# Performance work log

Measured on AMD Instinct MI355X. Metric: run time of the kernel, lower is better.

The kernel has to match this reference:

```python
import jax, jax.numpy as jnp
import numpy as np

N, D, H, C, E, I, L, B = 16000, 128, 2, 128, 256000, 512, 2, 64
NTYPES = 10


def setup_inputs() -> dict:
    key = jax.random.key(0)
    ks = jax.random.split(key, 20)
    s = 0.05
    inp = {
        'x': jax.random.normal(ks[0], (N, D), jnp.float32),
        'hetro_emb': jax.random.normal(ks[1], (NTYPES, D), jnp.float32) * s,
        'Wq': jax.random.normal(ks[2], (D, H * C), jnp.float32) * s,
        'bq': jnp.zeros((H * C,), jnp.float32),
        'Wk': jax.random.normal(ks[3], (D, H * C), jnp.float32) * s,
        'bk': jnp.zeros((H * C,), jnp.float32),
        'Wv': jax.random.normal(ks[4], (D, H * C), jnp.float32) * s,
        'bv': jnp.zeros((H * C,), jnp.float32),
        'We': jax.random.normal(ks[5], (D, H * C), jnp.float32) * s,
        'Wskip': jax.random.normal(ks[6], (D, C), jnp.float32) * s,
        'bskip': jnp.zeros((C,), jnp.float32),
        'ln_gamma': jnp.ones((L, D), jnp.float32),
        'ln_beta': jnp.zeros((L, D), jnp.float32),
        'ffn_w1': jax.random.normal(ks[7], (L, D, I), jnp.float32) * s,
        'ffn_b1': jnp.zeros((L, I), jnp.float32),
        'ffn_w2': jax.random.normal(ks[8], (L, I, D), jnp.float32) * s,
        'ffn_b2': jnp.zeros((L, D), jnp.float32),
        'edge_index': jax.random.randint(ks[9], (2, E), 0, N, jnp.int64),
        'edge_type': jax.random.randint(ks[10], (E,), 0, NTYPES, jnp.int64),
        'mask_idx': jax.random.randint(ks[11], (B,), 0, N, jnp.int64),
    }
    return inp


def _layer_norm(h, gamma, beta, eps=1e-6):
    mu = h.mean(-1, keepdims=True)
    var = ((h - mu) ** 2).mean(-1, keepdims=True)
    return (h - mu) * jax.lax.rsqrt(var + eps) * gamma + beta


def reference(x, hetro_emb, Wq, bq, Wk, bk, Wv, bv, We, Wskip, bskip,
              ln_gamma, ln_beta, ffn_w1, ffn_b1, ffn_w2, ffn_b2,
              edge_index, edge_type, mask_idx):
    src, dst = edge_index[0], edge_index[1]  # messages flow src(j) -> dst(i)
    edge_attr_raw = hetro_emb[edge_type]     # [E, D], computed once outside the layer loop
    scale = 1.0 / jnp.sqrt(jnp.asarray(C, x.dtype))

    h = x
    pre = h
    for l in range(L):
        # shared GRANConv weights across layers (same module appended n_gcn_layer times)
        q = (h @ Wq + bq).reshape(-1, H, C)
        k = (h @ Wk + bk).reshape(-1, H, C)
        v = (h @ Wv + bv).reshape(-1, H, C)
        eproj = (edge_attr_raw @ We).reshape(-1, H, C)  # [E, H, C]
        kj = k[src] + eproj                              # [E, H, C]
        logits = (q[dst] * kj).sum(-1) * scale           # [E, H]
        # segment softmax over destination nodes
        m = jax.ops.segment_max(logits, dst, num_segments=N)  # [N, H]
        a = jnp.exp(logits - m[dst])
        ssum = jax.ops.segment_sum(a, dst, num_segments=N)
        alpha = a / (ssum[dst] + 1e-16)                  # [E, H]
        msg = (v[src] + eproj) * alpha[..., None]        # [E, H, C]
        agg = jax.ops.segment_sum(msg, dst, num_segments=N)  # [N, H, C]
        out = agg.mean(1) + (h @ Wskip + bskip)          # concat=False -> head mean; root skip
        # residual + LN + FFN (no activation between the two FFN linears)
        hres = out + pre
        hln = _layer_norm(hres, ln_gamma[l], ln_beta[l])
        h = (hln @ ffn_w1[l] + ffn_b1[l]) @ ffn_w2[l] + ffn_b2[l]
        pre = h

    return h[mask_idx]  # [B, D]
```

## Files before the change

kernel.cpp:

```cpp
#include <hip/hip_runtime.h>
#include <hip/hip_bf16.h>
#include <math.h>

#define DD 128
#define QW 896
#define CAP 128
#define NB 125
#define BCAP 4096

typedef _Float16 f16x8 __attribute__((ext_vector_type(8)));
typedef _Float16 f16x2 __attribute__((ext_vector_type(2)));
typedef float f32x4 __attribute__((ext_vector_type(4)));

__device__ __forceinline__ float fdot2f(f16x2 a, f16x2 b, float c) {
#if __has_builtin(__builtin_amdgcn_fdot2)
  return __builtin_amdgcn_fdot2(a, b, c, false);
#else
  return fmaf((float)a[0], (float)b[0], fmaf((float)a[1], (float)b[1], c));
#endif
}

__global__ __launch_bounds__(256) void csr_count(const int* __restrict__ edst,
                                                 int* __restrict__ bcnt, int E) {
  __shared__ int h[NB];
  const int tid = threadIdx.x;
  if (tid < NB) h[tid] = 0;
  __syncthreads();
  const int e0 = blockIdx.x * 2048;
  for (int k = 0; k < 8; ++k) {
    int e = e0 + k * 256 + tid;
    if (e < E) atomicAdd(&h[edst[e] >> 7], 1);
  }
  __syncthreads();
  if (tid < NB && h[tid]) atomicAdd(&bcnt[tid], h[tid]);
}

__global__ __launch_bounds__(128) void csr_scan(const int* __restrict__ bcnt,
                                                int* __restrict__ bbase,
                                                int* __restrict__ bcursor,
                                                int* __restrict__ offs, int E, int Nn) {
  __shared__ int sc[128];
  const int tid = threadIdx.x;
  sc[tid] = (tid < NB) ? bcnt[tid] : 0;
  __syncthreads();
  for (int d = 1; d < 128; d <<= 1) {
    int t = (tid >= d) ? sc[tid - d] : 0;
    __syncthreads();
    sc[tid] += t;
    __syncthreads();
  }
  const int excl = tid ? sc[tid - 1] : 0;
  if (tid < NB) { bbase[tid] = excl; bcursor[tid] = excl; }
  if (tid == 0) { bbase[NB] = E; offs[Nn] = E; }
}

__global__ __launch_bounds__(256) void csr_scatter(const int* __restrict__ edst,
                                                   const int* __restrict__ esrc,
                                                   const int* __restrict__ etyp,
                                                   int* __restrict__ bcursor,
                                                   unsigned* __restrict__ ebuf, int E) {
  __shared__ int h[NB], cur[NB];
  const int tid = threadIdx.x;
  if (tid < NB) h[tid] = 0;
  __syncthreads();
  const int e0 = blockIdx.x * 2048;
  int dd[8];
  for (int k = 0; k < 8; ++k) {
    int e = e0 + k * 256 + tid;
    dd[k] = (e < E) ? edst[e] : -1;
    if (dd[k] >= 0) atomicAdd(&h[dd[k] >> 7], 1);
  }
  __syncthreads();
  if (tid < NB && h[tid]) cur[tid] = atomicAdd(&bcursor[tid], h[tid]);
  __syncthreads();
  for (int k = 0; k < 8; ++k) {
    int e = e0 + k * 256 + tid;
    if (dd[k] >= 0) {
      int pos = atomicAdd(&cur[dd[k] >> 7], 1);
      ebuf[pos] = (unsigned)esrc[e] | ((unsigned)etyp[e] << 14) |
                  ((unsigned)(dd[k] & 127) << 18);
    }
  }
}

__global__ __launch_bounds__(256) void csr_fine(const unsigned* __restrict__ ebuf,
                                                const int* __restrict__ bbase,
                                                unsigned* __restrict__ epk,
                                                int* __restrict__ offs,
                                                int* __restrict__ dcnt) {
  __shared__ unsigned sed[BCAP];
  __shared__ unsigned sout[BCAP];
  __shared__ int fh[128], sc[128], fc[128], hb[64];
  const int b = blockIdx.x, tid = threadIdx.x;
  const int base = bbase[b], cnt = bbase[b + 1] - base;
  for (int idx = tid; idx < cnt; idx += 256) sed[idx] = ebuf[base + idx];
  if (tid < 128) fh[tid] = 0;
  if (tid < 64) hb[tid] = 0;
  __syncthreads();
  for (int idx = tid; idx < cnt; idx += 256) atomicAdd(&fh[(sed[idx] >> 18) & 127], 1);
  __syncthreads();
  if (tid < 128) sc[tid] = fh[tid];
  __syncthreads();
  for (int d = 1; d < 128; d <<= 1) {
    int t = (tid < 128 && tid >= d) ? sc[tid - d] : 0;
    __syncthreads();
    if (tid < 128) sc[tid] += t;
    __syncthreads();
  }
  if (tid < 128) {
    const int excl = tid ? sc[tid - 1] : 0;
    offs[b * 128 + tid] = base + excl;
    fc[tid] = excl;
    atomicAdd(&hb[min(fh[tid], 63)], 1);
  }
  __syncthreads();
  if (tid < 64 && hb[tid]) atomicAdd(&dcnt[tid], hb[tid]);
  for (int idx = tid; idx < cnt; idx += 256) {
    const unsigned v = sed[idx];
    const int pos = atomicAdd(&fc[(v >> 18) & 127], 1);
    sout[pos] = (v & 0x3FFF) | (((v >> 14) & 0xF) << 18);
  }
  __syncthreads();
  for (int idx = tid; idx < cnt; idx += 256) epk[base + idx] = sout[idx];
}

__global__ __launch_bounds__(64) void deg_scan(const int* __restrict__ dcnt,
                                               int* __restrict__ dcur) {
  const int t = threadIdx.x;
  int s = 0;
  for (int d = t + 1; d < 64; ++d) s += dcnt[d];
  dcur[t] = s;
}

__global__ __launch_bounds__(256) void deg_order(const int* __restrict__ offs,
                                                 int* __restrict__ dcur,
                                                 int* __restrict__ order, int Nn) {
  __shared__ int h[64], cbase[64];
  const int tid = threadIdx.x;
  const int i = blockIdx.x * 256 + tid;
  if (tid < 64) h[tid] = 0;
  __syncthreads();
  int bk = -1;
  if (i < Nn) {
    bk = min(offs[i + 1] - offs[i], 63);
    atomicAdd(&h[bk], 1);
  }
  __syncthreads();
  if (tid < 64) {
    const int c = h[tid];
    cbase[tid] = c ? atomicAdd(&dcur[tid], c) : 0;
    h[tid] = 0;
  }
  __syncthreads();
  if (bk >= 0) {
    const int pos = cbase[bk] + atomicAdd(&h[bk], 1);
    order[pos] = i;
  }
}

__global__ __launch_bounds__(256) void pp_cast(
    const float* __restrict__ Wq, const float* __restrict__ Wk,
    const float* __restrict__ Wv, const float* __restrict__ Wsk,
    const float* __restrict__ bq, const float* __restrict__ bk,
    const float* __restrict__ bv, const float* __restrict__ bsk,
    const float* __restrict__ hemb, const float* __restrict__ We,
    const float* __restrict__ x,
    const float* __restrict__ fw1, const float* __restrict__ fb1,
    const float* __restrict__ fw2, const float* __restrict__ fb2,
    _Float16* __restrict__ WcatT, float* __restrict__ Wcat, float* __restrict__ bcat,
    _Float16* __restrict__ epth, _Float16* __restrict__ xh,
    _Float16* __restrict__ fw1h,
    float* __restrict__ bfv, float* __restrict__ bzero, int Nn) {
  int t = blockIdx.x * 256 + threadIdx.x;
  if (t < 256) {
    int l = t >> 7, j = t & 127;
    const float* b1 = fb1 + l * 512;
    const float* w2 = fw2 + (size_t)l * 65536 + j;
    float s0 = fb2[l * 128 + j], s1 = 0.f, s2 = 0.f, s3 = 0.f;
    for (int k = 0; k < 512; k += 4) {
      s0 = fmaf(b1[k], w2[(size_t)k * 128], s0);
      s1 = fmaf(b1[k + 1], w2[(size_t)(k + 1) * 128], s1);
      s2 = fmaf(b1[k + 2], w2[(size_t)(k + 2) * 128], s2);
      s3 = fmaf(b1[k + 3], w2[(size_t)(k + 3) * 128], s3);
    }
    bfv[t] = ((s0 + s1) + (s2 + s3));
    return;
  }
  t -= 256;
  if (t < 2560) {
    int ty = t >> 8, col = t & 255;
    float s0 = 0.f, s1 = 0.f, s2 = 0.f, s3 = 0.f;
    const float* hr = hemb + ty * 128;
    for (int c = 0; c < 128; c += 4) {
      s0 = fmaf(hr[c], We[c * 256 + col], s0);
      s1 = fmaf(hr[c + 1], We[(c + 1) * 256 + col], s1);
      s2 = fmaf(hr[c + 2], We[(c + 2) * 256 + col], s2);
      s3 = fmaf(hr[c + 3], We[(c + 3) * 256 + col], s3);
    }
    epth[t] = (_Float16)((s0 + s1) + (s2 + s3));
    return;
  }
  t -= 2560;
  if (t < 114688) {
    int n = t >> 7, k = t & 127;
    float v;
    if (n < 256) v = Wq[k * 256 + n];
    else if (n < 512) v = Wk[k * 256 + (n - 256)];
    else if (n < 768) v = Wv[k * 256 + (n - 512)];
    else v = Wsk[k * 128 + (n - 768)];
    WcatT[t] = (_Float16)v;
    Wcat[k * 896 + n] = v;
    return;
  }
  t -= 114688;
  if (t < 896) {
    float v;
    if (t < 256) v = bq[t];
    else if (t < 512) v = bk[t - 256];
    else if (t < 768) v = bv[t - 512];
    else v = bsk[t - 768];
    bcat[t] = v;
    return;
  }
  t -= 896;
  if (t < 1024) { bzero[t] = 0.f; return; }
  t -= 1024;
  if (t < 16384) {
    float4 v0 = *reinterpret_cast<const float4*>(fw1 + (size_t)t * 8);
    float4 v1 = *reinterpret_cast<const float4*>(fw1 + (size_t)t * 8 + 4);
    f16x8 o;
    o[0] = (_Float16)v0.x; o[1] = (_Float16)v0.y; o[2] = (_Float16)v0.z; o[3] = (_Float16)v0.w;
    o[4] = (_Float16)v1.x; o[5] = (_Float16)v1.y; o[6] = (_Float16)v1.z; o[7] = (_Float16)v1.w;
    *reinterpret_cast<f16x8*>(fw1h + (size_t)t * 8) = o;
    return;
  }
  t -= 16384;
  if (t < Nn * 16) {
    float4 v0 = *reinterpret_cast<const float4*>(x + (size_t)t * 8);
    float4 v1 = *reinterpret_cast<const float4*>(x + (size_t)t * 8 + 4);
    f16x8 o;
    o[0] = (_Float16)v0.x; o[1] = (_Float16)v0.y; o[2] = (_Float16)v0.z; o[3] = (_Float16)v0.w;
    o[4] = (_Float16)v1.x; o[5] = (_Float16)v1.y; o[6] = (_Float16)v1.z; o[7] = (_Float16)v1.w;
    *reinterpret_cast<f16x8*>(xh + (size_t)t * 8) = o;
  }
}

__global__ __launch_bounds__(256) void tr_fw2(const float* __restrict__ fw2,
                                              _Float16* __restrict__ fw2Th) {
  __shared__ _Float16 tile[64][65];
  const int l = blockIdx.z;
  const int k0 = blockIdx.x * 64, j0 = blockIdx.y * 64;
  const size_t base = (size_t)l * 65536;
  const int tid = threadIdx.x;
  for (int idx = tid; idx < 4096; idx += 256) {
    int r = idx >> 6, c = idx & 63;
    tile[r][c] = (_Float16)fw2[base + (size_t)(k0 + r) * 128 + j0 + c];
  }
  __syncthreads();
  for (int idx = tid; idx < 4096; idx += 256) {
    int r = idx >> 6, c = idx & 63;
    fw2Th[base + (size_t)(j0 + r) * 512 + k0 + c] = tile[c][r];
  }
}

__global__ __launch_bounds__(256) void pp_bmid(const float* __restrict__ bfv,
                                               const float* __restrict__ Wcat,
                                               const float* __restrict__ bcat,
                                               float* __restrict__ bmid) {
  int t = blockIdx.x * 256 + threadIdx.x;
  if (t >= 1024) return;
  if (t < 128) { bmid[t] = bfv[t]; return; }
  int n = t - 128;
  float s0 = bcat[n], s1 = 0.f, s2 = 0.f, s3 = 0.f;
  for (int c = 0; c < 128; c += 4) {
    s0 = fmaf(bfv[c], Wcat[c * 896 + n], s0);
    s1 = fmaf(bfv[c + 1], Wcat[(c + 1) * 896 + n], s1);
    s2 = fmaf(bfv[c + 2], Wcat[(c + 2) * 896 + n], s2);
    s3 = fmaf(bfv[c + 3], Wcat[(c + 3) * 896 + n], s3);
  }
  bmid[t] = ((s0 + s1) + (s2 + s3));
}

__global__ __launch_bounds__(256) void wf_gemm(const _Float16* __restrict__ fw1h,
                                               const _Float16* __restrict__ fw2Th,
                                               float* __restrict__ Wf,
                                               _Float16* __restrict__ Wfh,
                                               _Float16* __restrict__ BtMid0) {
  const int z = blockIdx.z;
  const _Float16* A = fw1h + z * 65536;
  const _Float16* Bt = fw2Th + z * 65536;
  const int tid = threadIdx.x;
  const int wid = tid >> 6, lane = tid & 63;
  const int wr = wid >> 1, wc = wid & 1;
  const int il = lane & 15, g = lane >> 4;
  const int row0 = wr * 64, col0 = wc * 64;
  const _Float16* Ap = A + (size_t)(row0 + il) * 512 + 8 * g;
  const _Float16* Bp = Bt + (size_t)(col0 + il) * 512 + 8 * g;
  f32x4 acc[4][4];
#pragma unroll
  for (int a = 0; a < 4; ++a)
#pragma unroll
    for (int b = 0; b < 4; ++b) acc[a][b] = (f32x4){0.f, 0.f, 0.f, 0.f};
  for (int k0 = 0; k0 < 512; k0 += 32) {
    f16x8 af[4], bf[4];
#pragma unroll
    for (int f = 0; f < 4; ++f) {
      af[f] = *reinterpret_cast<const f16x8*>(Ap + (size_t)(f * 16) * 512 + k0);
      bf[f] = *reinterpret_cast<const f16x8*>(Bp + (size_t)(f * 16) * 512 + k0);
    }
#pragma unroll
    for (int fi = 0; fi < 4; ++fi)
#pragma unroll
      for (int fj = 0; fj < 4; ++fj)
        acc[fi][fj] = __builtin_amdgcn_mfma_f32_16x16x32_f16(af[fi], bf[fj], acc[fi][fj], 0, 0, 0);
  }
#pragma unroll
  for (int fj = 0; fj < 4; ++fj) {
    const int col = col0 + fj * 16 + il;
#pragma unroll
    for (int fi = 0; fi < 4; ++fi) {
#pragma unroll
      for (int i = 0; i < 4; ++i) {
        const int row = row0 + fi * 16 + g * 4 + i;
        const float v = acc[fi][fj][i];
        Wf[z * 16384 + row * 128 + col] = v;
        if (z == 0) {
          Wfh[row * 128 + col] = (_Float16)v;
          BtMid0[col * 128 + row] = (_Float16)v;
        }
      }
    }
  }
}

template <bool HAS_CFH, bool HAS_CH, bool HAS_CHT>
__global__ __launch_bounds__(256) void gemm_tn_f16(const _Float16* __restrict__ A,
                                                   const _Float16* __restrict__ Bt,
                                                   const float* __restrict__ bias,
                                                   _Float16* __restrict__ Cfh, int NF,
                                                   _Float16* __restrict__ Ch, int choff, int ldh,
                                                   _Float16* __restrict__ ChT, int ldt,
                                                   int M, int N, int K) {
  const int tid = threadIdx.x;
  const int wid = tid >> 6, lane = tid & 63;
  const int wr = wid >> 1, wc = wid & 1;
  const int il = lane & 15, g = lane >> 4;
  const int row0 = blockIdx.y * 128 + wr * 64;
  const int col0 = blockIdx.x * 128 + wc * 64;
  const _Float16* Ap = A + (size_t)(row0 + il) * K + 8 * g;
  const _Float16* Bp = Bt + (size_t)(col0 + il) * K + 8 * g;
  f32x4 acc[4][4];
#pragma unroll
  for (int a = 0; a < 4; ++a)
#pragma unroll
    for (int b = 0; b < 4; ++b) acc[a][b] = (f32x4){0.f, 0.f, 0.f, 0.f};
  for (int k0 = 0; k0 < K; k0 += 32) {
    f16x8 af[4], bf[4];
#pragma unroll
    for (int f = 0; f < 4; ++f) {
      af[f] = *reinterpret_cast<const f16x8*>(Ap + (size_t)(f * 16) * K + k0);
      bf[f] = *reinterpret_cast<const f16x8*>(Bp + (size_t)(f * 16) * K + k0);
    }
#pragma unroll
    for (int fi = 0; fi < 4; ++fi)
#pragma unroll
      for (int fj = 0; fj < 4; ++fj)
        acc[fi][fj] = __builtin_amdgcn_mfma_f32_16x16x32_f16(af[fi], bf[fj], acc[fi][fj], 0, 0, 0);
  }
#pragma unroll
  for (int fj = 0; fj < 4; ++fj) {
    const int col = col0 + fj * 16 + il;
    const float b = bias[col];
#pragma unroll
    for (int fi = 0; fi < 4; ++fi) {
#pragma unroll
      for (int i = 0; i < 4; ++i) {
        const int row = row0 + fi * 16 + g * 4 + i;
        const float v = acc[fi][fj][i] + b;
        if constexpr (HAS_CFH) { if (col < NF) Cfh[(size_t)row * NF + col] = (_Float16)v; }
        if constexpr (HAS_CH) { if (col >= choff) Ch[(size_t)row * ldh + (col - choff)] = (_Float16)v; }
        if constexpr (HAS_CHT) { ChT[(size_t)col * ldt + row] = (_Float16)v; }
      }
    }
  }
}

__global__ __launch_bounds__(256) void node_attn_ln_kernel(
    const _Float16* __restrict__ QKVSh, const _Float16* __restrict__ epth,
    const _Float16* __restrict__ hpre,
    const int* __restrict__ offs, const unsigned* __restrict__ epk,
    const int* __restrict__ order,
    const float* __restrict__ gamma, const float* __restrict__ beta,
    _Float16* __restrict__ hlnh, int Nn) {
  __shared__ float sl0[4][CAP], sl1[4][CAP];
  __shared__ unsigned spk[4][CAP];
  __shared__ float sqe[4][2][10];
  __shared__ __align__(16) _Float16 elds[2560];
  const int tid = threadIdx.x;
  for (int t = tid; t < 1280; t += 256)
    reinterpret_cast<unsigned*>(elds)[t] = reinterpret_cast<const unsigned*>(epth)[t];
  __syncthreads();
  const int w = tid >> 6, lane = tid & 63;
  const int i = order[blockIdx.x * 4 + w];
  const int sub = lane >> 5;
  const int r = lane & 31;
  const int half = r >> 4;
  const int co = r << 3;
  const float scale = 0.08838834764831845f;
  f16x8 qh = *reinterpret_cast<const f16x8*>(QKVSh + (size_t)i * QW + co);
  const f16x2* q2 = reinterpret_cast<const f16x2*>(&qh);
#pragma unroll
  for (int ty = 0; ty < 10; ++ty) {
    f16x8 ev = *reinterpret_cast<const f16x8*>(elds + (ty << 8) + co);
    const f16x2* e2 = reinterpret_cast<const f16x2*>(&ev);
    float s = 0.f;
#pragma unroll
    for (int p2 = 0; p2 < 4; ++p2) s = fdot2f(q2[p2], e2[p2], s);
    s += __shfl_xor(s, 1); s += __shfl_xor(s, 2);
    s += __shfl_xor(s, 4); s += __shfl_xor(s, 8);
    if (lane < 32 && (r & 15) == 0) sqe[w][half][ty] = s * scale;
  }
  __threadfence_block();
  float m_me = -1e30f, s_me = 0.f;
  float acc[8] = {0.f};
  const int ebeg = offs[i], eend = offs[i + 1];
  for (int cs = ebeg; cs < eend; cs += CAP) {
    const int cnt = min(CAP, eend - cs);
    const int last = cnt - 1;
    for (int j = lane; j < cnt; j += 64) spk[w][j] = epk[cs + j];
    __threadfence_block();
    float cmax = -1e30f;
    {
      unsigned pk0 = spk[w][min(sub, last)];
      unsigned pk1 = spk[w][min(2 + sub, last)];
      f16x8 kv0 = *reinterpret_cast<const f16x8*>(QKVSh + (size_t)(pk0 & 0x3FFFF) * QW + 256 + co);
      f16x8 kv1 = *reinterpret_cast<const f16x8*>(QKVSh + (size_t)(pk1 & 0x3FFFF) * QW + 256 + co);
      int ty0 = pk0 >> 18, ty1 = pk1 >> 18;
      for (int j = 0; j < cnt; j += 2) {
        f16x8 kc = kv0;
        const int tyc = ty0;
        kv0 = kv1; ty0 = ty1;
        unsigned pkn = spk[w][min(j + 4 + sub, last)];
        ty1 = pkn >> 18;
        kv1 = *reinterpret_cast<const f16x8*>(QKVSh + (size_t)(pkn & 0x3FFFF) * QW + 256 + co);
        const f16x2* k2 = reinterpret_cast<const f16x2*>(&kc);
        float d = 0.f;
#pragma unroll
        for (int p2 = 0; p2 < 4; ++p2) d = fdot2f(q2[p2], k2[p2], d);
        d += __shfl_xor(d, 1); d += __shfl_xor(d, 2);
        d += __shfl_xor(d, 4); d += __shfl_xor(d, 8);
        d = d * scale + sqe[w][half][tyc];
        if (j + sub < cnt) {
          cmax = fmaxf(cmax, d);
          if ((r & 15) == 0) (half ? sl1 : sl0)[w][j + sub] = d;
        }
      }
    }
    cmax = fmaxf(cmax, __shfl_xor(cmax, 32));
    const float nm = fmaxf(m_me, cmax);
    const float rr = __expf(m_me - nm);
    s_me *= rr;
#pragma unroll
    for (int t = 0; t < 8; ++t) acc[t] *= rr;
    m_me = nm;
    __threadfence_block();
    {
      unsigned pk0 = spk[w][min(sub, last)];
      unsigned pk1 = spk[w][min(2 + sub, last)];
      f16x8 vv0 = *reinterpret_cast<const f16x8*>(QKVSh + (size_t)(pk0 & 0x3FFFF) * QW + 512 + co);
      f16x8 ee0 = *reinterpret_cast<const f16x8*>(elds + ((pk0 >> 18) << 8) + co);
      f16x8 vv1 = *reinterpret_cast<const f16x8*>(QKVSh + (size_t)(pk1 & 0x3FFFF) * QW + 512 + co);
      f16x8 ee1 = *reinterpret_cast<const f16x8*>(elds + ((pk1 >> 18) << 8) + co);
      const float* slme = (half ? sl1 : sl0)[w];
      float ls = 0.f;
      for (int j = 0; j < cnt; j += 2) {
        f16x8 vc = vv0, ec = ee0;
        vv0 = vv1; ee0 = ee1;
        unsigned pkn = spk[w][min(j + 4 + sub, last)];
        vv1 = *reinterpret_cast<const f16x8*>(QKVSh + (size_t)(pkn & 0x3FFFF) * QW + 512 + co);
        ee1 = *reinterpret_cast<const f16x8*>(elds + ((pkn >> 18) << 8) + co);
        const int jc = j + sub;
        float e = 0.f;
        if (jc < cnt) e = __expf(slme[jc] - m_me);
        ls += e;
#pragma unroll
        for (int t = 0; t < 8; ++t) acc[t] = fmaf((float)vc[t] + (float)ec[t], e, acc[t]);
      }
      s_me += ls;
    }
  }
  const float s_tot = s_me + __shfl_xor(s_me, 32);
  const float invme = 1.f / (s_tot + 1e-16f);
  float g[8];
#pragma unroll
  for (int t = 0; t < 8; ++t) {
    float a = acc[t] + __shfl_xor(acc[t], 32);
    a *= invme;
    g[t] = 0.5f * (a + __shfl_xor(a, 16));
  }
  const int cm = (r & 15) << 3;
  f16x8 sk = *reinterpret_cast<const f16x8*>(QKVSh + (size_t)i * QW + 768 + cm);
  f16x8 pr = *reinterpret_cast<const f16x8*>(hpre + (size_t)i * DD + cm);
  float xv[8];
#pragma unroll
  for (int t = 0; t < 8; ++t) xv[t] = g[t] + (float)sk[t] + (float)pr[t];
  float sm = 0.f;
#pragma unroll
  for (int t = 0; t < 8; ++t) sm += xv[t];
  sm += __shfl_xor(sm, 1); sm += __shfl_xor(sm, 2);
  sm += __shfl_xor(sm, 4); sm += __shfl_xor(sm, 8);
  const float mu = sm * (1.f / 128.f);
  float dx[8], vvs = 0.f;
#pragma unroll
  for (int t = 0; t < 8; ++t) { dx[t] = xv[t] - mu; vvs += dx[t] * dx[t]; }
  vvs += __shfl_xor(vvs, 1); vvs += __shfl_xor(vvs, 2);
  vvs += __shfl_xor(vvs, 4); vvs += __shfl_xor(vvs, 8);
  const float rstd = rsqrtf(vvs * (1.f / 128.f) + 1e-6f);
  if (lane < 16) {
    float4 gm0 = *reinterpret_cast<const float4*>(gamma + cm);
    float4 gm1 = *reinterpret_cast<const float4*>(gamma + cm + 4);
    float4 bt0 = *reinterpret_cast<const float4*>(beta + cm);
    float4 bt1 = *reinterpret_cast<const float4*>(beta + cm + 4);
    f16x8 o;
    o[0] = (_Float16)(dx[0] * rstd * gm0.x + bt0.x);
    o[1] = (_Float16)(dx[1] * rstd * gm0.y + bt0.y);
    o[2] = (_Float16)(dx[2] * rstd * gm0.z + bt0.z);
    o[3] = (_Float16)(dx[3] * rstd * gm0.w + bt0.w);
    o[4] = (_Float16)(dx[4] * rstd * gm1.x + bt1.x);
    o[5] = (_Float16)(dx[5] * rstd * gm1.y + bt1.y);
    o[6] = (_Float16)(dx[6] * rstd * gm1.z + bt1.z);
    o[7] = (_Float16)(dx[7] * rstd * gm1.w + bt1.w);
    *reinterpret_cast<f16x8*>(hlnh + (size_t)i * DD + cm) = o;
  }
}

__global__ __launch_bounds__(128) void final_kernel(const _Float16* __restrict__ hlnh1,
                                                    const float* __restrict__ Wf,
                                                    const float* __restrict__ bfv,
                                                    const int* __restrict__ midx,
                                                    float* __restrict__ out) {
  __shared__ float rowv[128];
  const int b = blockIdx.x, j = threadIdx.x;
  const int row = midx[b];
  rowv[j] = (float)hlnh1[(size_t)row * DD + j];
  __syncthreads();
  const float* w1 = Wf + 16384 + j;
  float s = bfv[128 + j];
#pragma unroll 4
  for (int c = 0; c < 128; ++c) s = fmaf(rowv[c], w1[c * 128], s);
  out[b * DD + j] = s;
}

extern "C" void kernel_launch(void* const* d_in, const int* in_sizes, int n_in,
                              void* d_out, int out_size, void* d_ws, size_t ws_size,
                              hipStream_t stream) {
  const float* x    = (const float*)d_in[0];
  const float* hemb = (const float*)d_in[1];
  const float* Wq   = (const float*)d_in[2];
  const float* bq   = (const float*)d_in[3];
  const float* Wk   = (const float*)d_in[4];
  const float* bk   = (const float*)d_in[5];
  const float* Wv   = (const float*)d_in[6];
  const float* bv   = (const float*)d_in[7];
  const float* We   = (const float*)d_in[8];
  const float* Wsk  = (const float*)d_in[9];
  const float* bsk  = (const float*)d_in[10];
  const float* lng  = (const float*)d_in[11];
  const float* lnb  = (const float*)d_in[12];
  const float* fw1  = (const float*)d_in[13];
  const float* fb1  = (const float*)d_in[14];
  const float* fw2  = (const float*)d_in[15];
  const float* fb2  = (const float*)d_in[16];
  const int* eidx   = (const int*)d_in[17];
  const int* etyp   = (const int*)d_in[18];
  const int* midx   = (const int*)d_in[19];

  const int Nn = in_sizes[0] / DD;
  const int E = in_sizes[18];

  const int* esrc = eidx;
  const int* edst = eidx + E;

  char* p = (char*)d_ws;
  auto alloc = [&](size_t bytes) -> void* {
    void* r = (void*)p;
    p += (bytes + 255) & ~(size_t)255;
    return r;
  };
  _Float16* QKVSh = (_Float16*)alloc((size_t)Nn * QW * 2);
  _Float16* xh    = (_Float16*)alloc((size_t)Nn * DD * 2);
  _Float16* hln0  = (_Float16*)alloc((size_t)Nn * DD * 2);
  _Float16* hln1  = (_Float16*)alloc((size_t)Nn * DD * 2);
  _Float16* h1h   = (_Float16*)alloc((size_t)Nn * DD * 2);
  _Float16* WcatT = (_Float16*)alloc((size_t)QW * DD * 2);
  float*    Wcat  = (float*)alloc((size_t)DD * QW * 4);
  float*    bcat  = (float*)alloc(QW * 4);
  _Float16* epth  = (_Float16*)alloc(2560 * 2);
  _Float16* fw1h  = (_Float16*)alloc((size_t)2 * DD * 512 * 2);
  _Float16* fw2Th = (_Float16*)alloc((size_t)2 * DD * 512 * 2);
  float*    Wf    = (float*)alloc(2 * 128 * 128 * 4);
  _Float16* Wfh   = (_Float16*)alloc(128 * 128 * 2);
  float*    bfv   = (float*)alloc(256 * 4);
  float*    bzero = (float*)alloc(1024 * 4);
  _Float16* BtMid = (_Float16*)alloc((size_t)1024 * 128 * 2);
  float*    bmid  = (float*)alloc(1024 * 4);
  int* offs   = (int*)alloc((size_t)(Nn + 1) * 4);
  int* bcnt   = (int*)alloc((NB + 1) * 4);
  int* bbase  = (int*)alloc((NB + 1) * 4);
  int* bcursor= (int*)alloc((NB + 1) * 4);
  int* dcnt   = (int*)alloc(64 * 4);
  int* dcur   = (int*)alloc(64 * 4);
  int* order  = (int*)alloc((size_t)Nn * 4);
  unsigned* ebuf = (unsigned*)alloc((size_t)E * 4);
  unsigned* epk  = (unsigned*)alloc((size_t)E * 4);

  hipMemsetAsync(bcnt, 0, (NB + 1) * sizeof(int), stream);
  hipMemsetAsync(dcnt, 0, 64 * sizeof(int), stream);
  csr_count<<<(E + 2047) / 2048, 256, 0, stream>>>(edst, bcnt, E);
  csr_scan<<<1, 128, 0, stream>>>(bcnt, bbase, bcursor, offs, E, Nn);
  csr_scatter<<<(E + 2047) / 2048, 256, 0, stream>>>(edst, esrc, etyp, bcursor, ebuf, E);
  csr_fine<<<NB, 256, 0, stream>>>(ebuf, bbase, epk, offs, dcnt);
  deg_scan<<<1, 64, 0, stream>>>(dcnt, dcur);
  deg_order<<<(Nn + 255) / 256, 256, 0, stream>>>(offs, dcur, order, Nn);

  const int pc_threads = 256 + 2560 + 114688 + 896 + 1024 + 16384 + Nn * 16;
  pp_cast<<<(pc_threads + 255) / 256, 256, 0, stream>>>(
      Wq, Wk, Wv, Wsk, bq, bk, bv, bsk, hemb, We, x, fw1, fb1, fw2, fb2,
      WcatT, Wcat, bcat, epth, xh, fw1h, bfv, bzero, Nn);
  tr_fw2<<<dim3(8, 2, 2), 256, 0, stream>>>(fw2, fw2Th);
  pp_bmid<<<4, 256, 0, stream>>>(bfv, Wcat, bcat, bmid);
  wf_gemm<<<dim3(1, 1, 2), 256, 0, stream>>>(fw1h, fw2Th, Wf, Wfh, BtMid);
  gemm_tn_f16<false, false, true><<<dim3(7, 1), 256, 0, stream>>>(
      Wfh, WcatT, bzero, nullptr, 0, nullptr, 0, 0, BtMid + 16384, 128, 128, 896, 128);

  gemm_tn_f16<false, true, false><<<dim3(QW / 128, Nn / 128), 256, 0, stream>>>(
      xh, WcatT, bcat, nullptr, 0, QKVSh, 0, QW, nullptr, 0, Nn, QW, DD);
  node_attn_ln_kernel<<<Nn / 4, 256, 0, stream>>>(QKVSh, epth, xh, offs, epk, order,
                                                  lng, lnb, hln0, Nn);
  gemm_tn_f16<true, true, false><<<dim3(1024 / 128, Nn / 128), 256, 0, stream>>>(
      hln0, BtMid, bmid, h1h, 128, QKVSh, 128, QW, nullptr, 0, Nn, 1024, DD);
  node_attn_ln_kernel<<<Nn / 4, 256, 0, stream>>>(QKVSh, epth, h1h, offs, epk, order,
                                                  lng + DD, lnb + DD, hln1, Nn);
  final_kernel<<<64, 128, 0, stream>>>(hln1, Wf, bfv, midx, (float*)d_out);
}
```

Measured before the change: 257.4 us.

## Use single-pass online softmax in attention; drop memsets and fold transpose into cast kernel

The node attention kernel now runs a single-pass online softmax. It loads K and V together per edge straight from global memory and rescales lazily, replacing the two-pass chunked scheme that staged logits and packed edges in shared memory. The two half-waves' partial max/sum are merged with a rescale at the end. Separately, the global atomics and memsets for the bucket and degree counts become per-block partial arrays summed in the scan kernels, and the fw2 transpose kernel is folded into extra blocks of pp_cast, cutting launches. The risk is more divergent exponent and rescale work per edge, plus register pressure from prefetching both K and V.

New measurement: 274.9 us. +6.8%, slower.

```diff
diff --git a/kernel.cpp b/kernel.cpp
--- a/kernel.cpp
+++ b/kernel.cpp
@@ -4,7 +4,6 @@
 
 #define DD 128
 #define QW 896
-#define CAP 128
 #define NB 125
 #define BCAP 4096
 
@@ -21,7 +20,7 @@
 }
 
 __global__ __launch_bounds__(256) void csr_count(const int* __restrict__ edst,
-                                                 int* __restrict__ bcnt, int E) {
+                                                 int* __restrict__ bparts, int E) {
   __shared__ int h[NB];
   const int tid = threadIdx.x;
   if (tid < NB) h[tid] = 0;
@@ -32,16 +31,18 @@
     if (e < E) atomicAdd(&h[edst[e] >> 7], 1);
   }
   __syncthreads();
-  if (tid < NB && h[tid]) atomicAdd(&bcnt[tid], h[tid]);
-}
-
-__global__ __launch_bounds__(128) void csr_scan(const int* __restrict__ bcnt,
+  if (tid < 128) bparts[blockIdx.x * 128 + tid] = (tid < NB) ? h[tid] : 0;
+}
+
+__global__ __launch_bounds__(128) void csr_scan(const int* __restrict__ bparts, int nblk,
                                                 int* __restrict__ bbase,
                                                 int* __restrict__ bcursor,
                                                 int* __restrict__ offs, int E, int Nn) {
   __shared__ int sc[128];
   const int tid = threadIdx.x;
-  sc[tid] = (tid < NB) ? bcnt[tid] : 0;
+  int s = 0;
+  for (int b = 0; b < nblk; ++b) s += bparts[b * 128 + tid];
+  sc[tid] = (tid < NB) ? s : 0;
   __syncthreads();
   for (int d = 1; d < 128; d <<= 1) {
     int t = (tid >= d) ? sc[tid - d] : 0;
@@ -87,7 +88,7 @@
                                                 const int* __restrict__ bbase,
                                                 unsigned* __restrict__ epk,
                                                 int* __restrict__ offs,
-                                                int* __restrict__ dcnt) {
+                                                int* __restrict__ dparts) {
   __shared__ unsigned sed[BCAP];
   __shared__ unsigned sout[BCAP];
   __shared__ int fh[128], sc[128], fc[128], hb[64];
@@ -114,7 +115,7 @@
     atomicAdd(&hb[min(fh[tid], 63)], 1);
   }
   __syncthreads();
-  if (tid < 64 && hb[tid]) atomicAdd(&dcnt[tid], hb[tid]);
+  if (tid < 64) dparts[b * 64 + tid] = hb[tid];
   for (int idx = tid; idx < cnt; idx += 256) {
     const unsigned v = sed[idx];
     const int pos = atomicAdd(&fc[(v >> 18) & 127], 1);
@@ -124,12 +125,17 @@
   for (int idx = tid; idx < cnt; idx += 256) epk[base + idx] = sout[idx];
 }
 
-__global__ __launch_bounds__(64) void deg_scan(const int* __restrict__ dcnt,
+__global__ __launch_bounds__(64) void deg_scan(const int* __restrict__ dparts, int nblk,
                                                int* __restrict__ dcur) {
+  __shared__ int tot[64];
   const int t = threadIdx.x;
   int s = 0;
-  for (int d = t + 1; d < 64; ++d) s += dcnt[d];
-  dcur[t] = s;
+  for (int b = 0; b < nblk; ++b) s += dparts[b * 64 + t];
+  tot[t] = s;
+  __syncthreads();
+  int acc = 0;
+  for (int d = t + 1; d < 64; ++d) acc += tot[d];
+  dcur[t] = acc;
 }
 
 __global__ __launch_bounds__(256) void deg_order(const int* __restrict__ offs,
@@ -169,8 +175,26 @@
     const float* __restrict__ fw2, const float* __restrict__ fb2,
     _Float16* __restrict__ WcatT, float* __restrict__ Wcat, float* __restrict__ bcat,
     _Float16* __restrict__ epth, _Float16* __restrict__ xh,
-    _Float16* __restrict__ fw1h,
-    float* __restrict__ bfv, float* __restrict__ bzero, int Nn) {
+    _Float16* __restrict__ fw1h, _Float16* __restrict__ fw2Th,
+    float* __restrict__ bfv, float* __restrict__ bzero, int Nn, int nb0) {
+  __shared__ _Float16 tile[64][65];
+  if (blockIdx.x >= nb0) {
+    const int tb = blockIdx.x - nb0;
+    const int l = tb >> 4, r2 = tb & 15;
+    const int k0 = (r2 >> 1) << 6, j0 = (r2 & 1) << 6;
+    const size_t base = (size_t)l * 65536;
+    const int tid = threadIdx.x;
+    for (int idx = tid; idx < 4096; idx += 256) {
+      int rr = idx >> 6, cc = idx & 63;
+      tile[rr][cc] = (_Float16)fw2[base + (size_t)(k0 + rr) * 128 + j0 + cc];
+    }
+    __syncthreads();
+    for (int idx = tid; idx < 4096; idx += 256) {
+      int rr = idx >> 6, cc = idx & 63;
+      fw2Th[base + (size_t)(j0 + rr) * 512 + k0 + cc] = tile[cc][rr];
+    }
+    return;
+  }
   int t = blockIdx.x * 256 + threadIdx.x;
   if (t < 256) {
     int l = t >> 7, j = t & 127;
@@ -242,24 +266,6 @@
     o[0] = (_Float16)v0.x; o[1] = (_Float16)v0.y; o[2] = (_Float16)v0.z; o[3] = (_Float16)v0.w;
     o[4] = (_Float16)v1.x; o[5] = (_Float16)v1.y; o[6] = (_Float16)v1.z; o[7] = (_Float16)v1.w;
     *reinterpret_cast<f16x8*>(xh + (size_t)t * 8) = o;
-  }
-}
-
-__global__ __launch_bounds__(256) void tr_fw2(const float* __restrict__ fw2,
-                                              _Float16* __restrict__ fw2Th) {
-  __shared__ _Float16 tile[64][65];
-  const int l = blockIdx.z;
-  const int k0 = blockIdx.x * 64, j0 = blockIdx.y * 64;
-  const size_t base = (size_t)l * 65536;
-  const int tid = threadIdx.x;
-  for (int idx = tid; idx < 4096; idx += 256) {
-    int r = idx >> 6, c = idx & 63;
-    tile[r][c] = (_Float16)fw2[base + (size_t)(k0 + r) * 128 + j0 + c];
-  }
-  __syncthreads();
-  for (int idx = tid; idx < 4096; idx += 256) {
-    int r = idx >> 6, c = idx & 63;
-    fw2Th[base + (size_t)(j0 + r) * 512 + k0 + c] = tile[c][r];
   }
 }
 
@@ -392,8 +398,6 @@
     const int* __restrict__ order,
     const float* __restrict__ gamma, const float* __restrict__ beta,
     _Float16* __restrict__ hlnh, int Nn) {
-  __shared__ float sl0[4][CAP], sl1[4][CAP];
-  __shared__ unsigned spk[4][CAP];
   __shared__ float sqe[4][2][10];
   __shared__ __align__(16) _Float16 elds[2560];
   const int tid = threadIdx.x;
@@ -424,78 +428,63 @@
   float m_me = -1e30f, s_me = 0.f;
   float acc[8] = {0.f};
   const int ebeg = offs[i], eend = offs[i + 1];
-  for (int cs = ebeg; cs < eend; cs += CAP) {
-    const int cnt = min(CAP, eend - cs);
-    const int last = cnt - 1;
-    for (int j = lane; j < cnt; j += 64) spk[w][j] = epk[cs + j];
-    __threadfence_block();
-    float cmax = -1e30f;
-    {
-      unsigned pk0 = spk[w][min(sub, last)];
-      unsigned pk1 = spk[w][min(2 + sub, last)];
-      f16x8 kv0 = *reinterpret_cast<const f16x8*>(QKVSh + (size_t)(pk0 & 0x3FFFF) * QW + 256 + co);
-      f16x8 kv1 = *reinterpret_cast<const f16x8*>(QKVSh + (size_t)(pk1 & 0x3FFFF) * QW + 256 + co);
-      int ty0 = pk0 >> 18, ty1 = pk1 >> 18;
-      for (int j = 0; j < cnt; j += 2) {
-        f16x8 kc = kv0;
-        const int tyc = ty0;
-        kv0 = kv1; ty0 = ty1;
-        unsigned pkn = spk[w][min(j + 4 + sub, last)];
-        ty1 = pkn >> 18;
-        kv1 = *reinterpret_cast<const f16x8*>(QKVSh + (size_t)(pkn & 0x3FFFF) * QW + 256 + co);
-        const f16x2* k2 = reinterpret_cast<const f16x2*>(&kc);
-        float d = 0.f;
-#pragma unroll
-        for (int p2 = 0; p2 < 4; ++p2) d = fdot2f(q2[p2], k2[p2], d);
-        d += __shfl_xor(d, 1); d += __shfl_xor(d, 2);
-        d += __shfl_xor(d, 4); d += __shfl_xor(d, 8);
-        d = d * scale + sqe[w][half][tyc];
-        if (j + sub < cnt) {
-          cmax = fmaxf(cmax, d);
-          if ((r & 15) == 0) (half ? sl1 : sl0)[w][j + sub] = d;
-        }
+  if (ebeg < eend) {
+    const int last = eend - 1;
+    unsigned pk0 = epk[min(ebeg + sub, last)];
+    unsigned pk1 = epk[min(ebeg + 2 + sub, last)];
+    const _Float16* r0p = QKVSh + (size_t)(pk0 & 0x3FFFF) * QW;
+    const _Float16* r1p = QKVSh + (size_t)(pk1 & 0x3FFFF) * QW;
+    f16x8 kv0 = *reinterpret_cast<const f16x8*>(r0p + 256 + co);
+    f16x8 vv0 = *reinterpret_cast<const f16x8*>(r0p + 512 + co);
+    f16x8 kv1 = *reinterpret_cast<const f16x8*>(r1p + 256 + co);
+    f16x8 vv1 = *reinterpret_cast<const f16x8*>(r1p + 512 + co);
+    for (int j = ebeg; j < eend; j += 2) {
+      f16x8 kc = kv0, vc = vv0;
+      const unsigned pkc = pk0;
+      kv0 = kv1; vv0 = vv1; pk0 = pk1;
+      pk1 = epk[min(j + 4 + sub, last)];
+      const _Float16* rp = QKVSh + (size_t)(pk1 & 0x3FFFF) * QW;
+      kv1 = *reinterpret_cast<const f16x8*>(rp + 256 + co);
+      vv1 = *reinterpret_cast<const f16x8*>(rp + 512 + co);
+      const int tyc = pkc >> 18;
+      const f16x2* k2 = reinterpret_cast<const f16x2*>(&kc);
+      float d = 0.f;
+#pragma unroll
+      for (int p2 = 0; p2 < 4; ++p2) d = fdot2f(q2[p2], k2[p2], d);
+      d += __shfl_xor(d, 1); d += __shfl_xor(d, 2);
+      d += __shfl_xor(d, 4); d += __shfl_xor(d, 8);
+      d = d * scale + sqe[w][half][tyc];
+      float e;
+      if (d > m_me + 8.f) {
+        const float rr = __expf(m_me - d);
+        s_me *= rr;
+#pragma unroll
+        for (int t = 0; t < 8; ++t) acc[t] *= rr;
+        m_me = d;
+        e = 1.f;
+      } else {
+        e = __expf(d - m_me);
       }
-    }
-    cmax = fmaxf(cmax, __shfl_xor(cmax, 32));
-    const float nm = fmaxf(m_me, cmax);
-    const float rr = __expf(m_me - nm);
-    s_me *= rr;
-#pragma unroll
-    for (int t = 0; t < 8; ++t) acc[t] *= rr;
-    m_me = nm;
-    __threadfence_block();
-    {
-      unsigned pk0 = spk[w][min(sub, last)];
-      unsigned pk1 = spk[w][min(2 + sub, last)];
-      f16x8 vv0 = *reinterpret_cast<const f16x8*>(QKVSh + (size_t)(pk0 & 0x3FFFF) * QW + 512 + co);
-      f16x8 ee0 = *reinterpret_cast<const f16x8*>(elds + ((pk0 >> 18) << 8) + co);
-      f16x8 vv1 = *reinterpret_cast<const f16x8*>(QKVSh + (size_t)(pk1 & 0x3FFFF) * QW + 512 + co);
-      f16x8 ee1 = *reinterpret_cast<const f16x8*>(elds + ((pk1 >> 18) << 8) + co);
-      const float* slme = (half ? sl1 : sl0)[w];
-      float ls = 0.f;
-      for (int j = 0; j < cnt; j += 2) {
-        f16x8 vc = vv0, ec = ee0;
-        vv0 = vv1; ee0 = ee1;
-        unsigned pkn = spk[w][min(j + 4 + sub, last)];
-        vv1 = *reinterpret_cast<const f16x8*>(QKVSh + (size_t)(pkn & 0x3FFFF) * QW + 512 + co);
-        ee1 = *reinterpret_cast<const f16x8*>(elds + ((pkn >> 18) << 8) + co);
-        const int jc = j + sub;
-        float e = 0.f;
-        if (jc < cnt) e = __expf(slme[jc] - m_me);
-        ls += e;
-#pragma unroll
-        for (int t = 0; t < 8; ++t) acc[t] = fmaf((float)vc[t] + (float)ec[t], e, acc[t]);
-      }
-      s_me += ls;
-    }
-  }
-  const float s_tot = s_me + __shfl_xor(s_me, 32);
+      if (j + sub >= eend) e = 0.f;
+      s_me += e;
+      f16x8 ec = *reinterpret_cast<const f16x8*>(elds + (tyc << 8) + co);
+      f16x8 ve = vc + ec;
+#pragma unroll
+      for (int t = 0; t < 8; ++t) acc[t] = fmaf((float)ve[t], e, acc[t]);
+    }
+  }
+  const float mo = __shfl_xor(m_me, 32);
+  const float so = __shfl_xor(s_me, 32);
+  const float mf = fmaxf(m_me, mo);
+  const float sc_me = __expf(m_me - mf);
+  const float sc_o = __expf(mo - mf);
+  const float s_tot = s_me * sc_me + so * sc_o;
   const float invme = 1.f / (s_tot + 1e-16f);
   float g[8];
 #pragma unroll
   for (int t = 0; t < 8; ++t) {
-    float a = acc[t] + __shfl_xor(acc[t], 32);
-    a *= invme;
+    const float ao = __shfl_xor(acc[t], 32);
+    const float a = (acc[t] * sc_me + ao * sc_o) * invme;
     g[t] = 0.5f * (a + __shfl_xor(a, 16));
   }
   const int cm = (r & 15) << 3;
@@ -605,29 +594,28 @@
   _Float16* BtMid = (_Float16*)alloc((size_t)1024 * 128 * 2);
   float*    bmid  = (float*)alloc(1024 * 4);
   int* offs   = (int*)alloc((size_t)(Nn + 1) * 4);
-  int* bcnt   = (int*)alloc((NB + 1) * 4);
   int* bbase  = (int*)alloc((NB + 1) * 4);
   int* bcursor= (int*)alloc((NB + 1) * 4);
-  int* dcnt   = (int*)alloc(64 * 4);
   int* dcur   = (int*)alloc(64 * 4);
   int* order  = (int*)alloc((size_t)Nn * 4);
+  const int nsblk = (E + 2047) / 2048;
+  int* bparts = (int*)alloc((size_t)nsblk * 128 * 4);
+  int* dparts = (int*)alloc((size_t)NB * 64 * 4);
   unsigned* ebuf = (unsigned*)alloc((size_t)E * 4);
   unsigned* epk  = (unsigned*)alloc((size_t)E * 4);
 
-  hipMemsetAsync(bcnt, 0, (NB + 1) * sizeof(int), stream);
-  hipMemsetAsync(dcnt, 0, 64 * sizeof(int), stream);
-  csr_count<<<(E + 2047) / 2048, 256, 0, stream>>>(edst, bcnt, E);
-  csr_scan<<<1, 128, 0, stream>>>(bcnt, bbase, bcursor, offs, E, Nn);
-  csr_scatter<<<(E + 2047) / 2048, 256, 0, stream>>>(edst, esrc, etyp, bcursor, ebuf, E);
-  csr_fine<<<NB, 256, 0, stream>>>(ebuf, bbase, epk, offs, dcnt);
-  deg_scan<<<1, 64, 0, stream>>>(dcnt, dcur);
+  csr_count<<<nsblk, 256, 0, stream>>>(edst, bparts, E);
+  csr_scan<<<1, 128, 0, stream>>>(bparts, nsblk, bbase, bcursor, offs, E, Nn);
+  csr_scatter<<<nsblk, 256, 0, stream>>>(edst, esrc, etyp, bcursor, ebuf, E);
+  csr_fine<<<NB, 256, 0, stream>>>(ebuf, bbase, epk, offs, dparts);
+  deg_scan<<<1, 64, 0, stream>>>(dparts, NB, dcur);
   deg_order<<<(Nn + 255) / 256, 256, 0, stream>>>(offs, dcur, order, Nn);
 
   const int pc_threads = 256 + 2560 + 114688 + 896 + 1024 + 16384 + Nn * 16;
-  pp_cast<<<(pc_threads + 255) / 256, 256, 0, stream>>>(
+  const int nb0 = (pc_threads + 255) / 256;
+  pp_cast<<<nb0 + 32, 256, 0, stream>>>(
       Wq, Wk, Wv, Wsk, bq, bk, bv, bsk, hemb, We, x, fw1, fb1, fw2, fb2,
-      WcatT, Wcat, bcat, epth, xh, fw1h, bfv, bzero, Nn);
-  tr_fw2<<<dim3(8, 2, 2), 256, 0, stream>>>(fw2, fw2Th);
+      WcatT, Wcat, bcat, epth, xh, fw1h, fw2Th, bfv, bzero, Nn, nb0);
   pp_bmid<<<4, 256, 0, stream>>>(bfv, Wcat, bcat, bmid);
   wf_gemm<<<dim3(1, 1, 2), 256, 0, stream>>>(fw1h, fw2Th, Wf, Wfh, BtMid);
   gemm_tn_f16<false, false, true><<<dim3(7, 1), 256, 0, stream>>>(
```
